# Performance work log

Measured on AMD Instinct MI355X. Metric: run time of the kernel, lower is better.

Reference implementation:

```python
import jax, jax.numpy as jnp
import numpy as np

RADIUS = 0.05
HMIN = -0.02
HMAX = 0.04
NSAMPLE = 64


def setup_inputs() -> dict:
    key = jax.random.key(0)
    k1, k2, k3, k4 = jax.random.split(key, 4)
    B, N, P, C = 2, 16384, 1024, 256
    xyz = jax.random.uniform(k1, (B, N, 3), dtype=jnp.float32)
    new_xyz = jax.random.uniform(k2, (B, P, 3), dtype=jnp.float32)
    rot = jax.random.normal(k3, (B, P, 3, 3), dtype=jnp.float32)
    features = jax.random.normal(k4, (B, C, N), dtype=jnp.float32)
    return {"xyz": xyz, "new_xyz": new_xyz, "rot": rot, "features": features}


def cylinder_query(xyz, new_xyz, rot):
    """Returns (B, P, NSAMPLE) int32 indices into the N axis of xyz.

    Faithful to the torch version: the torch code sorts all N candidates by
    distance (knn with K=N) and then top-k's a cylinder score over them; since
    the candidate set is all N points, this equals a direct top-k of the score
    over N (candidate ordering only affects float ties).
    """
    # delta = candidate point - center, in world frame: (B, P, N, 3)
    delta = xyz[:, None, :, :] - new_xyz[:, :, None, :]
    # rotate into cylinder frame: matmul(delta, rot^T) -> sum_d delta_d * rot[j, d]
    dcyl = jnp.einsum('bpnd,bpjd->bpnj', delta, rot)
    x, y, z = dcyl[..., 0], dcyl[..., 1], dcyl[..., 2]
    radial = jnp.sqrt(jnp.maximum(y * y + z * z, 0.0))
    in_cyl = (radial <= RADIUS) & (x >= HMIN) & (x <= HMAX)
    score = jnp.where(in_cyl, radial + 1e-3 * jnp.abs(x), jnp.inf)
    # smallest-score top-k via top_k on negated score
    neg_vals, pos = jax.lax.top_k(-score, NSAMPLE)  # (B, P, NSAMPLE)
    vals = -neg_vals
    # fallback: nearest point (torch uses idx_cand[..., 0], the KNN-nearest)
    d2 = jnp.sum(delta * delta, axis=-1)  # (B, P, N)
    fallback = jnp.argmin(d2, axis=-1)  # (B, P)
    no_valid = jnp.isinf(vals[..., 0])  # no point inside cylinder
    idx = jnp.where(no_valid[..., None], fallback[..., None], pos)
    return idx


def reference(xyz, new_xyz, rot, features):
    B = xyz.shape[0]
    idx = cylinder_query(xyz, new_xyz, rot)  # (B, P, S)
    # group xyz: (B, P, S, 3)
    grouped_xyz = jax.vmap(lambda p, i: p[i])(xyz, idx)
    grouped_xyz = grouped_xyz - new_xyz[:, :, None, :]
    # rotate_xyz: grouped @ rot  -> sum_d g_d * rot[d, e]
    grouped_xyz = jnp.einsum('bpsd,bpde->bpse', grouped_xyz, rot)
    grouped_xyz = jnp.transpose(grouped_xyz, (0, 3, 1, 2))  # (B, 3, P, S)
    # group features: (B, C, P, S)
    grouped_feat = jax.vmap(lambda f, i: f[:, i])(features, idx)
    return jnp.concatenate([grouped_xyz, grouped_feat], axis=1)  # (B, 3+C, P, S)
```

## Files before the change

### kernel.cpp

```cpp
#include <hip/hip_runtime.h>
#include <stdint.h>

#define B_ 2
#define N_ 16384
#define P_ 1024
#define C_ 256
#define S_ 64
#define CH_ (C_ + 3)
#define CAP_ 512

#define INF_BITS 0x7F800000u

typedef unsigned long long u64;

struct QS {
    u64 keys[CAP_];
    uint32_t hist[4][256];
    u64 red[4];
    uint32_t wsum[4];
    int vflag[128];
    int cnt;
    int sel;
    uint32_t k;
};

struct GT {
    uint32_t tileu[32][130];
};

union USmem {
    QS qs;
    GT g;
};

__device__ __forceinline__ u64 umin64(u64 a, u64 b) { return a < b ? a : b; }

__device__ __forceinline__ uint32_t f2bf(float f) {
    uint32_t x = __float_as_uint(f);
    return (x + 0x7fffu + ((x >> 16) & 1u)) >> 16;
}
__device__ __forceinline__ float bf2f(uint32_t u) { return __uint_as_float(u << 16); }

__device__ u64 block_min_u64(u64 v, u64* s_red) {
    int tid = threadIdx.x;
#pragma unroll
    for (int o = 32; o > 0; o >>= 1)
        v = umin64(v, (u64)__shfl_xor(v, o, 64));
    __syncthreads();
    if ((tid & 63) == 0) s_red[tid >> 6] = v;
    __syncthreads();
    u64 r = s_red[0];
#pragma unroll
    for (int w = 1; w < 4; ++w) r = umin64(r, s_red[w]);
    return r;
}

__device__ __forceinline__ uint32_t eval_sb(float px, float py, float pz,
                                            float cx, float cy, float cz,
                                            float r0, float r1, float r2,
                                            float r3, float r4, float r5,
                                            float r6, float r7, float r8) {
    float dx = px - cx, dy = py - cy, dz = pz - cz;
    float xr = __fadd_rn(__fadd_rn(__fmul_rn(dx, r0), __fmul_rn(dy, r1)), __fmul_rn(dz, r2));
    float yr = __fadd_rn(__fadd_rn(__fmul_rn(dx, r3), __fmul_rn(dy, r4)), __fmul_rn(dz, r5));
    float zr = __fadd_rn(__fadd_rn(__fmul_rn(dx, r6), __fmul_rn(dy, r7)), __fmul_rn(dz, r8));
    float rad2 = __fadd_rn(__fmul_rn(yr, yr), __fmul_rn(zr, zr));
    float radial = __fsqrt_rn(fmaxf(rad2, 0.0f));
    bool valid = (radial <= 0.05f) && (xr >= -0.02f) && (xr <= 0.04f);
    float score = __fadd_rn(radial, __fmul_rn(1e-3f, fabsf(xr)));
    return valid ? __float_as_uint(score) : INF_BITS;
}

__device__ __forceinline__ uint32_t score_bits(const float* __restrict__ xb, int n,
                                               float cx, float cy, float cz,
                                               float r0, float r1, float r2,
                                               float r3, float r4, float r5,
                                               float r6, float r7, float r8) {
    return eval_sb(xb[n * 3 + 0], xb[n * 3 + 1], xb[n * 3 + 2],
                   cx, cy, cz, r0, r1, r2, r3, r4, r5, r6, r7, r8);
}

__device__ void select_idx(QS& qs, const float* __restrict__ xb,
                           float cx, float cy, float cz,
                           float r0, float r1, float r2, float r3, float r4,
                           float r5, float r6, float r7, float r8,
                           int* s_out) {
    const int tid = threadIdx.x;
    const int wid = tid >> 6;
    const int v = qs.cnt;

    if (v == 0) {
        u64 fb = ~0ull;
        for (int n = tid; n < N_; n += 256) {
            float px = xb[n * 3 + 0], py = xb[n * 3 + 1], pz = xb[n * 3 + 2];
            float dx = px - cx, dy = py - cy, dz = pz - cz;
            float d2 = __fadd_rn(__fadd_rn(__fmul_rn(dx, dx), __fmul_rn(dy, dy)),
                                 __fmul_rn(dz, dz));
            fb = umin64(fb, ((u64)__float_as_uint(d2) << 32) | (unsigned)n);
        }
        u64 m = block_min_u64(fb, qs.red);
        if (tid < S_) s_out[tid] = (int)(unsigned)(m & 0xFFFFFFFFu);
    } else if (v <= 64) {
        if (tid >= v && tid < 64)
            qs.keys[tid] = 0xFFFFFFFF00000000ull | (unsigned)(0x10000 + tid);
        __syncthreads();
        u64 key = 0;
        int rank = 0;
        if (tid < 64) {
            key = qs.keys[tid];
            for (int o = 0; o < 64; ++o) rank += (qs.keys[o] < key) ? 1 : 0;
        }
        __syncthreads();
        if (tid < 64) qs.keys[rank] = key;
        __syncthreads();
        const int needed = 64 - v;
        if (tid < 64 && needed > 0) {
            bool inv0 = (qs.vflag[tid] == 0);
            u64 m0 = __ballot(inv0);
            int before0 = __popcll(m0 & ((1ull << tid) - 1ull));
            if (inv0 && before0 < needed) qs.keys[v + before0] = (unsigned)tid;
            int c0 = __popcll(m0);
            if (c0 < needed) {
                bool inv1 = (qs.vflag[64 + tid] == 0);
                u64 m1 = __ballot(inv1);
                int b1 = c0 + __popcll(m1 & ((1ull << tid) - 1ull));
                if (inv1 && b1 < needed) qs.keys[v + b1] = (unsigned)(64 + tid);
            }
        }
        __syncthreads();
        if (tid < S_) s_out[tid] = (int)(unsigned)(qs.keys[tid] & 0xFFFFFFFFu);
    } else if (v <= CAP_) {
        for (int i = tid; i < v; i += 256) {
            u64 key = qs.keys[i];
            int rank = 0;
            for (int j = 0; j < v; ++j) rank += (qs.keys[j] < key) ? 1 : 0;
            if (rank < 64) s_out[rank] = (int)(unsigned)(key & 0xFFFFFFFFu);
        }
    } else {
        uint32_t prefix = 0, mask = 0, kk = 64;
        for (int pass = 0; pass < 4; ++pass) {
            const int shift = 24 - 8 * pass;
            __syncthreads();
            qs.hist[0][tid] = 0;
            qs.hist[1][tid] = 0;
            qs.hist[2][tid] = 0;
            qs.hist[3][tid] = 0;
            __syncthreads();
            for (int n = tid; n < N_; n += 256) {
                uint32_t sb = score_bits(xb, n, cx, cy, cz, r0, r1, r2, r3, r4, r5, r6, r7, r8);
                if (sb != INF_BITS && (sb & mask) == prefix)
                    atomicAdd(&qs.hist[wid][(sb >> shift) & 255u], 1u);
            }
            __syncthreads();
            uint32_t cnt = qs.hist[0][tid] + qs.hist[1][tid] + qs.hist[2][tid] + qs.hist[3][tid];
            uint32_t x = cnt;
#pragma unroll
            for (int o = 1; o < 64; o <<= 1) {
                uint32_t y = __shfl_up(x, o, 64);
                if ((tid & 63) >= o) x += y;
            }
            if ((tid & 63) == 63) qs.wsum[wid] = x;
            __syncthreads();
            uint32_t woff = 0;
            for (int w = 0; w < wid; ++w) woff += qs.wsum[w];
            uint32_t incl = x + woff;
            uint32_t excl = incl - cnt;
            if (kk > excl && kk <= incl) {
                qs.sel = tid;
                qs.k = kk - excl;
            }
            __syncthreads();
            prefix |= ((uint32_t)qs.sel) << shift;
            mask |= 255u << shift;
            kk = qs.k;
        }
        const uint32_t T = prefix;

        __syncthreads();
        if (tid == 0) qs.cnt = 0;
        __syncthreads();
        for (int n = tid; n < N_; n += 256) {
            uint32_t sb = score_bits(xb, n, cx, cy, cz, r0, r1, r2, r3, r4, r5, r6, r7, r8);
            if (sb != INF_BITS && sb <= T) {
                int pos = atomicAdd(&qs.cnt, 1);
                if (pos < CAP_) qs.keys[pos] = ((u64)sb << 32) | (unsigned)n;
            }
        }
        __syncthreads();
        int c = qs.cnt;
        if (c > CAP_) c = CAP_;
        for (int i = tid; i < c; i += 256) {
            u64 key = qs.keys[i];
            int rank = 0;
            for (int j = 0; j < c; ++j) rank += (qs.keys[j] < key) ? 1 : 0;
            if (rank < 64) s_out[rank] = (int)(unsigned)(key & 0xFFFFFFFFu);
        }
    }
}

__global__ __launch_bounds__(256) void transpose_kernel(const float* __restrict__ feat,
                                                        ushort* __restrict__ featT) {
    int t = blockIdx.x;
    int b = t >> 10;
    int rem = t & 1023;
    int cblk = rem >> 8;
    int nblk = rem & 255;
    __shared__ float tile[64][65];
    int tid = threadIdx.x;
    for (int i = tid; i < 64 * 64; i += 256) {
        int cy = i >> 6, nx = i & 63;
        tile[cy][nx] = feat[((size_t)(b * C_ + cblk * 64 + cy)) * N_ + nblk * 64 + nx];
    }
    __syncthreads();
    for (int i = tid; i < 64 * 32; i += 256) {
        int ny = i >> 5, cp = i & 31;
        uint32_t u0 = f2bf(tile[2 * cp + 0][ny]);
        uint32_t u1 = f2bf(tile[2 * cp + 1][ny]);
        *(uint32_t*)&featT[((size_t)(b * N_ + nblk * 64 + ny)) * C_ + cblk * 64 + 2 * cp] =
            u0 | (u1 << 16);
    }
}

__global__ __launch_bounds__(256) void qg_kernel(const ushort* __restrict__ featT,
                                                 const float* __restrict__ features,
                                                 const float* __restrict__ xyz,
                                                 const float* __restrict__ new_xyz,
                                                 const float* __restrict__ rot,
                                                 float* __restrict__ out, int useT) {
    __shared__ USmem sm;
    __shared__ int s_idx[S_];
    const int tid = threadIdx.x;
    const int lane = tid & 63;
    const int bp = blockIdx.x;
    const int b = bp >> 10;
    const int p = bp & 1023;

    if (tid == 0) sm.qs.cnt = 0;

    const float cx = new_xyz[bp * 3 + 0];
    const float cy = new_xyz[bp * 3 + 1];
    const float cz = new_xyz[bp * 3 + 2];
    const float* R = rot + (size_t)bp * 9;
    const float r0 = R[0], r1 = R[1], r2 = R[2];
    const float r3 = R[3], r4 = R[4], r5 = R[5];
    const float r6 = R[6], r7 = R[7], r8 = R[8];

    __syncthreads();

    const float* xb = xyz + (size_t)b * N_ * 3;
    const float4* xb4 = (const float4*)xb;

    for (int it = 0; it < N_ / 1024; ++it) {
        int t4 = it * 256 + tid;
        float4 A = xb4[t4 * 3 + 0];
        float4 Bv = xb4[t4 * 3 + 1];
        float4 Cv = xb4[t4 * 3 + 2];
        int n0 = t4 * 4;

        uint32_t s0 = eval_sb(A.x, A.y, A.z, cx, cy, cz, r0, r1, r2, r3, r4, r5, r6, r7, r8);
        uint32_t s1 = eval_sb(A.w, Bv.x, Bv.y, cx, cy, cz, r0, r1, r2, r3, r4, r5, r6, r7, r8);
        uint32_t s2 = eval_sb(Bv.z, Bv.w, Cv.x, cx, cy, cz, r0, r1, r2, r3, r4, r5, r6, r7, r8);
        uint32_t s3 = eval_sb(Cv.y, Cv.z, Cv.w, cx, cy, cz, r0, r1, r2, r3, r4, r5, r6, r7, r8);

        if (it == 0 && tid < 32) {
            sm.qs.vflag[n0 + 0] = (s0 != INF_BITS) ? 1 : 0;
            sm.qs.vflag[n0 + 1] = (s1 != INF_BITS) ? 1 : 0;
            sm.qs.vflag[n0 + 2] = (s2 != INF_BITS) ? 1 : 0;
            sm.qs.vflag[n0 + 3] = (s3 != INF_BITS) ? 1 : 0;
        }
        uint32_t mn = min(min(s0, s1), min(s2, s3));
        if (__any(mn != INF_BITS)) {
            uint32_t sb[4] = {s0, s1, s2, s3};
#pragma unroll
            for (int j = 0; j < 4; ++j) {
                u64 m = __ballot(sb[j] != INF_BITS);
                if (m) {
                    int leader = __builtin_ctzll(m);
                    int cnt = __popcll(m);
                    int base = 0;
                    if (lane == leader) base = atomicAdd(&sm.qs.cnt, cnt);
                    base = __shfl(base, leader, 64);
                    if (sb[j] != INF_BITS) {
                        int pos = base + __popcll(m & ((1ull << lane) - 1ull));
                        if (pos < CAP_) sm.qs.keys[pos] = ((u64)sb[j] << 32) | (unsigned)(n0 + j);
                    }
                }
            }
        }
    }
    __syncthreads();

    select_idx(sm.qs, xb, cx, cy, cz, r0, r1, r2, r3, r4, r5, r6, r7, r8, s_idx);
    __syncthreads();

    if (tid < S_) {
        int n = s_idx[tid];
        const float* pt = xyz + ((size_t)b * N_ + n) * 3;
        float dx = pt[0] - cx;
        float dy = pt[1] - cy;
        float dz = pt[2] - cz;
        float g0 = __fadd_rn(__fadd_rn(__fmul_rn(dx, r0), __fmul_rn(dy, r3)), __fmul_rn(dz, r6));
        float g1 = __fadd_rn(__fadd_rn(__fmul_rn(dx, r1), __fmul_rn(dy, r4)), __fmul_rn(dz, r7));
        float g2 = __fadd_rn(__fadd_rn(__fmul_rn(dx, r2), __fmul_rn(dy, r5)), __fmul_rn(dz, r8));
        out[(((size_t)b * CH_ + 0) * P_ + p) * S_ + tid] = g0;
        out[(((size_t)b * CH_ + 1) * P_ + p) * S_ + tid] = g1;
        out[(((size_t)b * CH_ + 2) * P_ + p) * S_ + tid] = g2;
    }

    for (int h = 0; h < 2; ++h) {
        if (h) __syncthreads();
        if (useT) {
            for (int i = tid; i < 32 * 64; i += 256) {
                int sl = i >> 6, cd = i & 63;
                int n = s_idx[h * 32 + sl];
                uint2 v = *(const uint2*)&featT[((size_t)b * N_ + n) * C_ + cd * 4];
                *(uint2*)&sm.g.tileu[sl][cd * 2] = v;
            }
        } else {
            for (int i = tid; i < 32 * 128; i += 256) {
                int sl = i >> 7, cp = i & 127;
                int n = s_idx[h * 32 + sl];
                uint32_t u0 = f2bf(features[((size_t)b * C_ + 2 * cp + 0) * N_ + n]);
                uint32_t u1 = f2bf(features[((size_t)b * C_ + 2 * cp + 1) * N_ + n]);
                sm.g.tileu[sl][cp] = u0 | (u1 << 16);
            }
        }
        __syncthreads();
        for (int i = tid; i < (C_ / 2) * 8; i += 256) {
            int cp = i >> 3, q = i & 7;
            uint32_t u0 = sm.g.tileu[4 * q + 0][cp];
            uint32_t u1 = sm.g.tileu[4 * q + 1][cp];
            uint32_t u2 = sm.g.tileu[4 * q + 2][cp];
            uint32_t u3 = sm.g.tileu[4 * q + 3][cp];
            float4 lo, hi;
            lo.x = bf2f(u0 & 0xffffu); lo.y = bf2f(u1 & 0xffffu);
            lo.z = bf2f(u2 & 0xffffu); lo.w = bf2f(u3 & 0xffffu);
            hi.x = bf2f(u0 >> 16); hi.y = bf2f(u1 >> 16);
            hi.z = bf2f(u2 >> 16); hi.w = bf2f(u3 >> 16);
            size_t base0 = (((size_t)b * CH_ + 3 + 2 * cp) * P_ + p) * S_ + h * 32 + 4 * q;
            *(float4*)&out[base0] = lo;
            *(float4*)&out[base0 + (size_t)P_ * S_] = hi;
        }
    }
}

extern "C" void kernel_launch(void* const* d_in, const int* in_sizes, int n_in,
                              void* d_out, int out_size, void* d_ws, size_t ws_size,
                              hipStream_t stream) {
    const float* xyz = (const float*)d_in[0];
    const float* new_xyz = (const float*)d_in[1];
    const float* rot = (const float*)d_in[2];
    const float* features = (const float*)d_in[3];
    float* out = (float*)d_out;

    const size_t featT_bytes = (size_t)B_ * N_ * C_ * sizeof(ushort);
    const int useT = (ws_size >= featT_bytes) ? 1 : 0;

    ushort* featT = (ushort*)d_ws;

    if (useT) {
        transpose_kernel<<<2048, 256, 0, stream>>>(features, featT);
    }
    qg_kernel<<<B_ * P_, 256, 0, stream>>>(featT, features, xyz, new_xyz, rot, out, useT);
}
```

Baseline: 65.80 us.

## Fuse feature transpose into query kernel and split gather into separate kernel

Merges the feature transpose into the cylinder-query kernel, with even blocks transposing before the query and odd blocks after it. The aim is to overlap the memory-bound transpose with the compute-bound query. The feature gather moves to a new group_kernel that reads indices written to workspace, since it needs the fully transposed features. This adds a second launch and an index round trip through global memory. If the workspace is too small for the transposed features, the index buffer is still written to the workspace unchecked.

```diff
diff --git a/kernel.cpp b/kernel.cpp
--- a/kernel.cpp
+++ b/kernel.cpp
@@ -24,13 +24,9 @@
     uint32_t k;
 };
 
-struct GT {
-    uint32_t tileu[32][130];
-};
-
-union USmem {
+union U1 {
+    float ttile[64][65];
     QS qs;
-    GT g;
 };
 
 __device__ __forceinline__ u64 umin64(u64 a, u64 b) { return a < b ? a : b; }
@@ -136,6 +132,7 @@
             for (int j = 0; j < v; ++j) rank += (qs.keys[j] < key) ? 1 : 0;
             if (rank < 64) s_out[rank] = (int)(unsigned)(key & 0xFFFFFFFFu);
         }
+        __syncthreads();
     } else {
         uint32_t prefix = 0, mask = 0, kk = 64;
         for (int pass = 0; pass < 4; ++pass) {
@@ -195,47 +192,49 @@
             for (int j = 0; j < c; ++j) rank += (qs.keys[j] < key) ? 1 : 0;
             if (rank < 64) s_out[rank] = (int)(unsigned)(key & 0xFFFFFFFFu);
         }
+        __syncthreads();
     }
 }
 
-__global__ __launch_bounds__(256) void transpose_kernel(const float* __restrict__ feat,
-                                                        ushort* __restrict__ featT) {
-    int t = blockIdx.x;
-    int b = t >> 10;
-    int rem = t & 1023;
-    int cblk = rem >> 8;
-    int nblk = rem & 255;
-    __shared__ float tile[64][65];
-    int tid = threadIdx.x;
-    for (int i = tid; i < 64 * 64; i += 256) {
-        int cy = i >> 6, nx = i & 63;
-        tile[cy][nx] = feat[((size_t)(b * C_ + cblk * 64 + cy)) * N_ + nblk * 64 + nx];
-    }
-    __syncthreads();
-    for (int i = tid; i < 64 * 32; i += 256) {
-        int ny = i >> 5, cp = i & 31;
-        uint32_t u0 = f2bf(tile[2 * cp + 0][ny]);
-        uint32_t u1 = f2bf(tile[2 * cp + 1][ny]);
-        *(uint32_t*)&featT[((size_t)(b * N_ + nblk * 64 + ny)) * C_ + cblk * 64 + 2 * cp] =
-            u0 | (u1 << 16);
-    }
-}
-
-__global__ __launch_bounds__(256) void qg_kernel(const ushort* __restrict__ featT,
-                                                 const float* __restrict__ features,
+__global__ __launch_bounds__(256) void tq_kernel(const float* __restrict__ feat,
+                                                 ushort* __restrict__ featT,
                                                  const float* __restrict__ xyz,
                                                  const float* __restrict__ new_xyz,
                                                  const float* __restrict__ rot,
+                                                 int* __restrict__ idx_out,
                                                  float* __restrict__ out, int useT) {
-    __shared__ USmem sm;
+    __shared__ U1 sm;
     __shared__ int s_idx[S_];
     const int tid = threadIdx.x;
     const int lane = tid & 63;
     const int bp = blockIdx.x;
     const int b = bp >> 10;
     const int p = bp & 1023;
-
-    if (tid == 0) sm.qs.cnt = 0;
+    const bool tfirst = ((blockIdx.x & 1) == 0);
+
+    auto transpose_phase = [&]() {
+        __syncthreads();
+        int t = blockIdx.x;
+        int tb = t >> 10;
+        int rem = t & 1023;
+        int cblk = rem >> 8;
+        int nblk = rem & 255;
+        for (int i = tid; i < 64 * 64; i += 256) {
+            int cy = i >> 6, nx = i & 63;
+            sm.ttile[cy][nx] = feat[((size_t)(tb * C_ + cblk * 64 + cy)) * N_ + nblk * 64 + nx];
+        }
+        __syncthreads();
+        for (int i = tid; i < 64 * 32; i += 256) {
+            int ny = i >> 5, cp = i & 31;
+            uint32_t u0 = f2bf(sm.ttile[2 * cp + 0][ny]);
+            uint32_t u1 = f2bf(sm.ttile[2 * cp + 1][ny]);
+            *(uint32_t*)&featT[((size_t)(tb * N_ + nblk * 64 + ny)) * C_ + cblk * 64 + 2 * cp] =
+                u0 | (u1 << 16);
+        }
+        __syncthreads();
+    };
+
+    if (useT && tfirst) transpose_phase();
 
     const float cx = new_xyz[bp * 3 + 0];
     const float cy = new_xyz[bp * 3 + 1];
@@ -245,6 +244,7 @@
     const float r3 = R[3], r4 = R[4], r5 = R[5];
     const float r6 = R[6], r7 = R[7], r8 = R[8];
 
+    if (tid == 0) sm.qs.cnt = 0;
     __syncthreads();
 
     const float* xb = xyz + (size_t)b * N_ * 3;
@@ -295,6 +295,7 @@
 
     if (tid < S_) {
         int n = s_idx[tid];
+        idx_out[(size_t)bp * S_ + tid] = n;
         const float* pt = xyz + ((size_t)b * N_ + n) * 3;
         float dx = pt[0] - cx;
         float dy = pt[1] - cy;
@@ -307,6 +308,23 @@
         out[(((size_t)b * CH_ + 2) * P_ + p) * S_ + tid] = g2;
     }
 
+    if (useT && !tfirst) transpose_phase();
+}
+
+__global__ __launch_bounds__(256) void group_kernel(const ushort* __restrict__ featT,
+                                                    const float* __restrict__ features,
+                                                    const int* __restrict__ idx,
+                                                    float* __restrict__ out, int useT) {
+    __shared__ uint32_t tileu[32][130];
+    __shared__ int s_idx[S_];
+    const int tid = threadIdx.x;
+    const int bp = blockIdx.x;
+    const int b = bp >> 10;
+    const int p = bp & 1023;
+
+    if (tid < S_) s_idx[tid] = idx[(size_t)bp * S_ + tid];
+    __syncthreads();
+
     for (int h = 0; h < 2; ++h) {
         if (h) __syncthreads();
         if (useT) {
@@ -314,7 +332,7 @@
                 int sl = i >> 6, cd = i & 63;
                 int n = s_idx[h * 32 + sl];
                 uint2 v = *(const uint2*)&featT[((size_t)b * N_ + n) * C_ + cd * 4];
-                *(uint2*)&sm.g.tileu[sl][cd * 2] = v;
+                *(uint2*)&tileu[sl][cd * 2] = v;
             }
         } else {
             for (int i = tid; i < 32 * 128; i += 256) {
@@ -322,16 +340,16 @@
                 int n = s_idx[h * 32 + sl];
                 uint32_t u0 = f2bf(features[((size_t)b * C_ + 2 * cp + 0) * N_ + n]);
                 uint32_t u1 = f2bf(features[((size_t)b * C_ + 2 * cp + 1) * N_ + n]);
-                sm.g.tileu[sl][cp] = u0 | (u1 << 16);
+                tileu[sl][cp] = u0 | (u1 << 16);
             }
         }
         __syncthreads();
         for (int i = tid; i < (C_ / 2) * 8; i += 256) {
             int cp = i >> 3, q = i & 7;
-            uint32_t u0 = sm.g.tileu[4 * q + 0][cp];
-            uint32_t u1 = sm.g.tileu[4 * q + 1][cp];
-            uint32_t u2 = sm.g.tileu[4 * q + 2][cp];
-            uint32_t u3 = sm.g.tileu[4 * q + 3][cp];
+            uint32_t u0 = tileu[4 * q + 0][cp];
+            uint32_t u1 = tileu[4 * q + 1][cp];
+            uint32_t u2 = tileu[4 * q + 2][cp];
+            uint32_t u3 = tileu[4 * q + 3][cp];
             float4 lo, hi;
             lo.x = bf2f(u0 & 0xffffu); lo.y = bf2f(u1 & 0xffffu);
             lo.z = bf2f(u2 & 0xffffu); lo.w = bf2f(u3 & 0xffffu);
@@ -354,12 +372,12 @@
     float* out = (float*)d_out;
 
     const size_t featT_bytes = (size_t)B_ * N_ * C_ * sizeof(ushort);
-    const int useT = (ws_size >= featT_bytes) ? 1 : 0;
+    const size_t idx_bytes = (size_t)B_ * P_ * S_ * sizeof(int);
+    const int useT = (ws_size >= featT_bytes + idx_bytes) ? 1 : 0;
 
     ushort* featT = (ushort*)d_ws;
-
-    if (useT) {
-        transpose_kernel<<<2048, 256, 0, stream>>>(features, featT);
-    }
-    qg_kernel<<<B_ * P_, 256, 0, stream>>>(featT, features, xyz, new_xyz, rot, out, useT);
-}
+    int* idx = useT ? (int*)((char*)d_ws + featT_bytes) : (int*)d_ws;
+
+    tq_kernel<<<B_ * P_, 256, 0, stream>>>(features, featT, xyz, new_xyz, rot, idx, out, useT);
+    group_kernel<<<B_ * P_, 256, 0, stream>>>(featT, features, idx, out, useT);
+}
```

Result: slower. 72.27 us (+9.8%).
